# Kernel optimization log

Measured on AMD Instinct MI355X. Metric: run time of the kernel, lower is better.

The kernel has to match this reference:

```python
import jax, jax.numpy as jnp
import numpy as np

N = 64        # SSM state size
L = 4096      # sequence / kernel length (l_max)
BH = 4096     # batch * channels


def setup_inputs() -> dict:
    key = jax.random.key(0)
    ks = jax.random.split(key, 8)
    u = jax.random.normal(ks[0], (BH, L), dtype=jnp.float32)
    # S4D-Lin style eigenvalue init: Re = -0.5, Im = pi * n
    Lambda_re = -0.5 * jnp.ones((N,), dtype=jnp.float32)
    Lambda_im = jnp.pi * jnp.arange(N, dtype=jnp.float32)
    P_re = jax.random.normal(ks[1], (N,), dtype=jnp.float32) * (0.5 ** 0.5)
    P_im = jax.random.normal(ks[2], (N,), dtype=jnp.float32) * (0.5 ** 0.5)
    B_re = jax.random.normal(ks[3], (N,), dtype=jnp.float32)
    B_im = jax.random.normal(ks[4], (N,), dtype=jnp.float32)
    C_ri = jax.random.normal(ks[5], (N, 2), dtype=jnp.float32) * (0.5 ** 0.5)
    D = jnp.ones((1,), dtype=jnp.float32)
    # log_step ~ uniform(log(0.001), log(0.1)) as in log_step_initializer
    log_step = jax.random.uniform(ks[6], (1,), dtype=jnp.float32,
                                  minval=jnp.log(0.001), maxval=jnp.log(0.1))
    return {"u": u, "Lambda_re": Lambda_re, "Lambda_im": Lambda_im,
            "P_re": P_re, "P_im": P_im, "B_re": B_re, "B_im": B_im,
            "C_ri": C_ri, "D": D, "log_step": log_step}


def kernel_DPLR(Lambda, P, Q, B, C, step, length):
    # Evaluate the SSM generating function at the roots of unity via 4 Cauchy dots,
    # then inverse FFT to recover the length-L convolution kernel.
    Omega_L = jnp.exp((-2j * jnp.pi) * (jnp.arange(length) / length))  # (L,)
    a0, a1 = jnp.conj(C), jnp.conj(Q)
    b0, b1 = B, P
    g = (2.0 / step) * ((1.0 - Omega_L) / (1.0 + Omega_L))  # (L,)
    c = 2.0 / (1.0 + Omega_L)                               # (L,)

    def cauchy(v):  # v: (N,) -> (L,)
        return (v[None, :] / (g[:, None] - Lambda[None, :])).sum(-1)

    k00 = cauchy(a0 * b0)
    k01 = cauchy(a0 * b1)
    k10 = cauchy(a1 * b0)
    k11 = cauchy(a1 * b1)
    at_roots = c * (k00 - k01 * (1.0 / (1.0 + k11)) * k10)
    return jnp.fft.ifft(at_roots, length).real  # (L,)


def causal_convolution(u, K):
    # FFT-based linear (causal) convolution; u: (..., L), K: (L,)
    n = 2 * u.shape[-1]
    ud = jnp.fft.rfft(u, n=n, axis=-1)
    Kd = jnp.fft.rfft(K, n=n)
    return jnp.fft.irfft(ud * Kd, n=n, axis=-1)[..., : u.shape[-1]]


def reference(u, Lambda_re, Lambda_im, P_re, P_im, B_re, B_im, C_ri, D, log_step):
    Lambda = Lambda_re + 1j * Lambda_im
    P = P_re + 1j * P_im
    B = B_re + 1j * B_im
    C = C_ri[..., 0] + 1j * C_ri[..., 1]
    step = jnp.exp(log_step)  # (1,)
    K = kernel_DPLR(Lambda, P, P, B, C, step, u.shape[-1])  # (L,) real
    y_s = causal_convolution(u, K) + D * u  # (BH, L)
    return y_s
```

## Files before the change

### kernel.cpp

```cpp
#include <hip/hip_runtime.h>
#include <math.h>

#define LSEQ 4096
#define MFFT 8192
#define NM   64
#define NBH  4096

__device__ __forceinline__ float2 cmulf(float2 a, float2 b) {
  return make_float2(a.x*b.x - a.y*b.y, a.x*b.y + a.y*b.x);
}
__device__ __forceinline__ float2 cmulc(float2 a, float2 b) {
  return make_float2(a.x*b.x + a.y*b.y, a.y*b.x - a.x*b.y);
}
__device__ __forceinline__ float2 caddf(float2 a, float2 b){ return make_float2(a.x+b.x, a.y+b.y); }
__device__ __forceinline__ float2 csubf(float2 a, float2 b){ return make_float2(a.x-b.x, a.y-b.y); }

__device__ __forceinline__ int ZS(int i){ return i ^ ((i>>4)&15) ^ (((i>>8)&15)<<4); }

__device__ __forceinline__ void dft8_fwd(float2 x[8]) {
  const float RC = 0.7071067811865476f;
  float2 u0=caddf(x[0],x[4]), v0=csubf(x[0],x[4]);
  float2 u1=caddf(x[1],x[5]), d1=csubf(x[1],x[5]);
  float2 u2=caddf(x[2],x[6]), d2=csubf(x[2],x[6]);
  float2 u3=caddf(x[3],x[7]), d3=csubf(x[3],x[7]);
  float2 v1 = make_float2(RC*(d1.x + d1.y), RC*(d1.y - d1.x));
  float2 v2 = make_float2(d2.y, -d2.x);
  float2 v3 = make_float2(RC*(d3.y - d3.x), -RC*(d3.x + d3.y));
  float2 p0=caddf(u0,u2), q0=csubf(u0,u2);
  float2 p1=caddf(u1,u3), qt=csubf(u1,u3);
  float2 q1 = make_float2(qt.y, -qt.x);
  float2 r0=caddf(v0,v2), s0=csubf(v0,v2);
  float2 r1=caddf(v1,v3), st=csubf(v1,v3);
  float2 s1 = make_float2(st.y, -st.x);
  x[0]=caddf(p0,p1); x[4]=csubf(p0,p1);
  x[2]=caddf(q0,q1); x[6]=csubf(q0,q1);
  x[1]=caddf(r0,r1); x[5]=csubf(r0,r1);
  x[3]=caddf(s0,s1); x[7]=csubf(s0,s1);
}
__device__ __forceinline__ void dft8_inv(float2 x[8]) {
  const float RC = 0.7071067811865476f;
  float2 p0=caddf(x[0],x[4]), p1=csubf(x[0],x[4]);
  float2 q0=caddf(x[2],x[6]), q1=csubf(x[2],x[6]);
  float2 r0=caddf(x[1],x[5]), r1=csubf(x[1],x[5]);
  float2 s0=caddf(x[3],x[7]), s1=csubf(x[3],x[7]);
  float2 q1i = make_float2(-q1.y, q1.x);
  float2 s1i = make_float2(-s1.y, s1.x);
  float2 u0=caddf(p0,q0), u2=csubf(p0,q0);
  float2 u1=caddf(p1,q1i), u3=csubf(p1,q1i);
  float2 v0=caddf(r0,s0), v2=csubf(r0,s0);
  float2 v1=caddf(r1,s1i), v3=csubf(r1,s1i);
  float2 w1 = make_float2(RC*(v1.x - v1.y), RC*(v1.x + v1.y));
  float2 w2 = make_float2(-v2.y, v2.x);
  float2 w3 = make_float2(-RC*(v3.x + v3.y), RC*(v3.x - v3.y));
  x[0]=caddf(u0,v0); x[4]=csubf(u0,v0);
  x[1]=caddf(u1,w1); x[5]=csubf(u1,w1);
  x[2]=caddf(u2,w2); x[6]=csubf(u2,w2);
  x[3]=caddf(u3,w3); x[7]=csubf(u3,w3);
}

__device__ __forceinline__ void tw_fwd(float2 x[8], const float4* __restrict__ T, int J, int j) {
  float4 a0 = T[j],       a1 = T[J+j];
  x[1]=cmulf(x[1],make_float2(a0.x,a0.y));
  x[2]=cmulf(x[2],make_float2(a0.z,a0.w));
  x[3]=cmulf(x[3],make_float2(a1.x,a1.y));
  x[4]=cmulf(x[4],make_float2(a1.z,a1.w));
  float4 a2 = T[2*J+j],   a3 = T[3*J+j];
  x[5]=cmulf(x[5],make_float2(a2.x,a2.y));
  x[6]=cmulf(x[6],make_float2(a2.z,a2.w));
  x[7]=cmulf(x[7],make_float2(a3.x,a3.y));
}
__device__ __forceinline__ void tw_inv(float2 x[8], const float4* __restrict__ T, int J, int j) {
  float4 a0 = T[j],       a1 = T[J+j];
  x[1]=cmulc(x[1],make_float2(a0.x,a0.y));
  x[2]=cmulc(x[2],make_float2(a0.z,a0.w));
  x[3]=cmulc(x[3],make_float2(a1.x,a1.y));
  x[4]=cmulc(x[4],make_float2(a1.z,a1.w));
  float4 a2 = T[2*J+j],   a3 = T[3*J+j];
  x[5]=cmulc(x[5],make_float2(a2.x,a2.y));
  x[6]=cmulc(x[6],make_float2(a2.z,a2.w));
  x[7]=cmulc(x[7],make_float2(a3.x,a3.y));
}

#define DECL_W16C \
  const float2 W16C[8] = { make_float2(1.f,0.f), \
    make_float2(0.9238795325112867f,-0.3826834323650898f), \
    make_float2(0.7071067811865476f,-0.7071067811865476f), \
    make_float2(0.3826834323650898f,-0.9238795325112867f), \
    make_float2(0.f,-1.f), \
    make_float2(-0.3826834323650898f,-0.9238795325112867f), \
    make_float2(-0.7071067811865476f,-0.7071067811865476f), \
    make_float2(-0.9238795325112867f,-0.3826834323650898f) };

__device__ __forceinline__ float2 W8192e(long long e) {
  double ang = -2.0*M_PI*(double)(e & (MFFT-1))/(double)MFFT;
  return make_float2((float)cos(ang), (float)sin(ang));
}

__global__ void prep1_kernel(const float* __restrict__ Lre, const float* __restrict__ Lim,
                             const float* __restrict__ Pre, const float* __restrict__ Pim,
                             const float* __restrict__ Bre, const float* __restrict__ Bim,
                             const float* __restrict__ Cri, const float* __restrict__ lstep,
                             float2* __restrict__ a_out,
                             float4* __restrict__ T1, float4* __restrict__ T2,
                             float4* __restrict__ T3) {
  if (blockIdx.x >= 64) {
    int idx = (blockIdx.x - 64)*blockDim.x + threadIdx.x;
    if (idx < 4096) {
      int q = idx >> 10, j = idx & 1023;
      float2 wa = W8192e((long long)j*(2*q+1));
      float2 wb = W8192e((long long)j*(2*q+2));
      T1[(q<<10)+j] = make_float4(wa.x, wa.y, wb.x, wb.y);
    } else if (idx < 4608) {
      int r = idx - 4096; int q = r >> 7, j = r & 127;
      float2 wa = W8192e(8LL*j*(2*q+1));
      float2 wb = W8192e(8LL*j*(2*q+2));
      T2[(q<<7)+j] = make_float4(wa.x, wa.y, wb.x, wb.y);
    } else if (idx < 4672) {
      int r = idx - 4608; int q = r >> 4, j = r & 15;
      float2 wa = W8192e(64LL*j*(2*q+1));
      float2 wb = W8192e(64LL*j*(2*q+2));
      T3[(q<<4)+j] = make_float4(wa.x, wa.y, wb.x, wb.y);
    }
    return;
  }
  const int tid = threadIdx.x;
  const int k = (blockIdx.x << 6) + (tid >> 2);
  const int sub = tid & 3;
  double step = exp((double)lstep[0]);
  double ang = -2.0*M_PI*(double)k/(double)LSEQ;
  double wr = cos(ang), wi = sin(ang);
  double nr = 1.0 - wr, ni = -wi;
  double dr = 1.0 + wr, di = wi;
  double dn = dr*dr + di*di;
  double gre = (2.0/step) * (nr*dr + ni*di)/dn;
  double gim = (2.0/step) * (ni*dr - nr*di)/dn;
  double cre = 2.0*dr/dn, cim = -2.0*di/dn;
  double k00r=0,k00i=0,k01r=0,k01i=0,k10r=0,k10i=0,k11r=0,k11i=0;
  for (int n = sub; n < NM; n += 4) {
    double lre = Lre[n], lim = Lim[n];
    double pre = Pre[n], pim = Pim[n];
    double bre = Bre[n], bim = Bim[n];
    double ccr = Cri[2*n], cci = Cri[2*n+1];
    double er = gre - lre, ei = gim - lim;
    double inv = 1.0/(er*er + ei*ei);
    double ir =  er*inv, ii = -ei*inv;
    double v00r = ccr*bre + cci*bim, v00i = ccr*bim - cci*bre;
    double v01r = ccr*pre + cci*pim, v01i = ccr*pim - cci*pre;
    double v10r = pre*bre + pim*bim, v10i = pre*bim - pim*bre;
    double v11r = pre*pre + pim*pim, v11i = 0.0;
    k00r += v00r*ir - v00i*ii;  k00i += v00r*ii + v00i*ir;
    k01r += v01r*ir - v01i*ii;  k01i += v01r*ii + v01i*ir;
    k10r += v10r*ir - v10i*ii;  k10i += v10r*ii + v10i*ir;
    k11r += v11r*ir - v11i*ii;  k11i += v11r*ii + v11i*ir;
  }
  #pragma unroll
  for (int d = 1; d <= 2; d <<= 1) {
    k00r += __shfl_xor(k00r, d);  k00i += __shfl_xor(k00i, d);
    k01r += __shfl_xor(k01r, d);  k01i += __shfl_xor(k01i, d);
    k10r += __shfl_xor(k10r, d);  k10i += __shfl_xor(k10i, d);
    k11r += __shfl_xor(k11r, d);  k11i += __shfl_xor(k11i, d);
  }
  if (sub == 0) {
    double numr = k01r*k10r - k01i*k10i, numi = k01r*k10i + k01i*k10r;
    double der = 1.0 + k11r, dei = k11i;
    double dinv = 1.0/(der*der + dei*dei);
    double qr = (numr*der + numi*dei)*dinv;
    double qi = (numi*der - numr*dei)*dinv;
    double tr = k00r - qr, ti = k00i - qi;
    double ar = cre*tr - cim*ti, ai = cre*ti + cim*tr;
    a_out[k] = make_float2((float)ar, (float)ai);
  }
}

__global__ void ktime_kernel(const float2* __restrict__ a, float* __restrict__ K) {
  int lane = threadIdx.x & 63;
  int l = blockIdx.x * (blockDim.x >> 6) + (threadIdx.x >> 6);
  if (l >= LSEQ) return;
  double ang0 = 2.0*M_PI*(double)((l*lane) & (LSEQ-1))/(double)LSEQ;
  double tr = cos(ang0), ti = sin(ang0);
  double ang1 = 2.0*M_PI*(double)(l & 63)/64.0;
  double wr = cos(ang1), wi = sin(ang1);
  double acc = 0.0;
  for (int k = 0; k < 64; k++) {
    float2 ak = a[lane + (k << 6)];
    acc += (double)ak.x*tr - (double)ak.y*ti;
    double ntr = tr*wr - ti*wi;
    ti = tr*wi + ti*wr;
    tr = ntr;
  }
  for (int off = 32; off > 0; off >>= 1) acc += __shfl_down(acc, off);
  if (lane == 0) K[l] = (float)(acc/(double)LSEQ);
}

__global__ void kd8_kernel(const float* __restrict__ K, const float* __restrict__ Dp,
                           const float4* __restrict__ T1, const float4* __restrict__ T2,
                           const float4* __restrict__ T3,
                           float2* __restrict__ KdE, float2* __restrict__ KdO) {
  __shared__ float2 z[MFFT];
  const int t = threadIdx.x;
  float2 x[8];
  #pragma unroll
  for (int k = 0; k < 4; k++) {
    float v = K[t + (k<<10)];
    if (t == 0 && k == 0) v += Dp[0];
    x[k] = make_float2(v, 0.f);
  }
  #pragma unroll
  for (int k = 4; k < 8; k++) x[k] = make_float2(0.f, 0.f);
  dft8_fwd(x); tw_fwd(x, T1, 1024, t);
  #pragma unroll
  for (int m = 0; m < 8; m++) z[ZS(t + (m<<10))] = x[m];
  __syncthreads();
  {
    const int j2 = t & 127, gb2 = (t>>7)<<10;
    int ai[8];
    #pragma unroll
    for (int m = 0; m < 8; m++) ai[m] = ZS(gb2 + j2 + (m<<7));
    #pragma unroll
    for (int m = 0; m < 8; m++) x[m] = z[ai[m]];
    dft8_fwd(x); tw_fwd(x, T2, 128, j2);
    #pragma unroll
    for (int m = 0; m < 8; m++) z[ai[m]] = x[m];
  }
  __syncthreads();
  {
    const int j3 = t & 15, gb3 = (t>>4)<<7;
    int ai[8];
    #pragma unroll
    for (int m = 0; m < 8; m++) ai[m] = ZS(gb3 + j3 + (m<<4));
    #pragma unroll
    for (int m = 0; m < 8; m++) x[m] = z[ai[m]];
    dft8_fwd(x); tw_fwd(x, T3, 16, j3);
    #pragma unroll
    for (int m = 0; m < 8; m++) z[ai[m]] = x[m];
  }
  __builtin_amdgcn_wave_barrier();
  {
    DECL_W16C
    const int G4 = t>>1, j1 = t & 1, gb4 = G4<<4;
    #pragma unroll
    for (int m = 0; m < 8; m++) x[m] = z[ZS(gb4 + j1 + (m<<1))];
    dft8_fwd(x);
    #pragma unroll
    for (int m = 1; m < 8; m++) {
      float2 wm = j1 ? W16C[m] : make_float2(1.f, 0.f);
      x[m] = cmulf(x[m], wm);
    }
    const float sc = 1.0f/8192.0f;
    float2* kout = (j1 ? KdO : KdE) + (G4<<3);
    #pragma unroll
    for (int p = 0; p < 8; p++) {
      float ox = __shfl_xor(x[p].x, 1);
      float oy = __shfl_xor(x[p].y, 1);
      float2 v = j1 ? make_float2(ox - x[p].x, oy - x[p].y)
                    : make_float2(x[p].x + ox, x[p].y + oy);
      kout[p] = make_float2(v.x*sc, v.y*sc);
    }
  }
}

__global__ __launch_bounds__(1024, 4)
void conv8_kernel(const float* __restrict__ u,
                  const float4* __restrict__ T1, const float4* __restrict__ T2,
                  const float4* __restrict__ T3,
                  const float2* __restrict__ KdE, const float2* __restrict__ KdO,
                  float* __restrict__ out) {
  __shared__ float2 z[MFFT];
  const int t = threadIdx.x;
  const int r0 = blockIdx.x, r1 = blockIdx.x + (NBH/2);
  const float* u0 = u + (size_t)r0*LSEQ;
  const float* u1 = u + (size_t)r1*LSEQ;
  float2 x[8];
  {
    #pragma unroll
    for (int k = 0; k < 4; k++)
      x[k] = make_float2(u0[t + (k<<10)], u1[t + (k<<10)]);
    #pragma unroll
    for (int k = 4; k < 8; k++) x[k] = make_float2(0.f, 0.f);
    dft8_fwd(x); tw_fwd(x, T1, 1024, t);
    #pragma unroll
    for (int m = 0; m < 8; m++) z[ZS(t + (m<<10))] = x[m];
  }
  __syncthreads();
  const int j2 = t & 127, gb2 = (t>>7)<<10;
  {
    int ai[8];
    #pragma unroll
    for (int m = 0; m < 8; m++) ai[m] = ZS(gb2 + j2 + (m<<7));
    #pragma unroll
    for (int m = 0; m < 8; m++) x[m] = z[ai[m]];
    dft8_fwd(x); tw_fwd(x, T2, 128, j2);
    #pragma unroll
    for (int m = 0; m < 8; m++) z[ai[m]] = x[m];
  }
  __syncthreads();
  const int j3 = t & 15, gb3 = (t>>4)<<7;
  {
    int ai[8];
    #pragma unroll
    for (int m = 0; m < 8; m++) ai[m] = ZS(gb3 + j3 + (m<<4));
    #pragma unroll
    for (int m = 0; m < 8; m++) x[m] = z[ai[m]];
    dft8_fwd(x); tw_fwd(x, T3, 16, j3);
    #pragma unroll
    for (int m = 0; m < 8; m++) z[ai[m]] = x[m];
  }
  __builtin_amdgcn_wave_barrier();
  {
    DECL_W16C
    const int G4 = t>>1, j1 = t & 1, gb4 = G4<<4;
    int ai[8];
    #pragma unroll
    for (int m = 0; m < 8; m++) ai[m] = ZS(gb4 + j1 + (m<<1));
    #pragma unroll
    for (int m = 0; m < 8; m++) x[m] = z[ai[m]];
    dft8_fwd(x);
    #pragma unroll
    for (int m = 1; m < 8; m++) {
      float2 wm = j1 ? W16C[m] : make_float2(1.f, 0.f);
      x[m] = cmulf(x[m], wm);
    }
    const float4* kp = (const float4*)((j1 ? KdO : KdE) + (G4<<3));
    #pragma unroll
    for (int p2 = 0; p2 < 4; p2++) {
      float4 kq = kp[p2];
      #pragma unroll
      for (int s = 0; s < 2; s++) {
        const int p = 2*p2 + s;
        float2 kd = s ? make_float2(kq.z, kq.w) : make_float2(kq.x, kq.y);
        float ox = __shfl_xor(x[p].x, 1);
        float oy = __shfl_xor(x[p].y, 1);
        float2 v = j1 ? make_float2(ox - x[p].x, oy - x[p].y)
                      : make_float2(x[p].x + ox, x[p].y + oy);
        x[p] = cmulf(v, kd);
      }
    }
    #pragma unroll
    for (int p = 0; p < 8; p++) {
      float ox = __shfl_xor(x[p].x, 1);
      float oy = __shfl_xor(x[p].y, 1);
      x[p] = j1 ? make_float2(ox - x[p].x, oy - x[p].y)
                : make_float2(x[p].x + ox, x[p].y + oy);
    }
    #pragma unroll
    for (int m = 1; m < 8; m++) {
      float2 wm = j1 ? W16C[m] : make_float2(1.f, 0.f);
      x[m] = cmulc(x[m], wm);
    }
    dft8_inv(x);
    #pragma unroll
    for (int m = 0; m < 8; m++) z[ai[m]] = x[m];
  }
  __builtin_amdgcn_wave_barrier();
  {
    int ai[8];
    #pragma unroll
    for (int m = 0; m < 8; m++) ai[m] = ZS(gb3 + j3 + (m<<4));
    #pragma unroll
    for (int m = 0; m < 8; m++) x[m] = z[ai[m]];
    tw_inv(x, T3, 16, j3); dft8_inv(x);
    #pragma unroll
    for (int m = 0; m < 8; m++) z[ai[m]] = x[m];
  }
  __syncthreads();
  {
    int ai[8];
    #pragma unroll
    for (int m = 0; m < 8; m++) ai[m] = ZS(gb2 + j2 + (m<<7));
    #pragma unroll
    for (int m = 0; m < 8; m++) x[m] = z[ai[m]];
    tw_inv(x, T2, 128, j2); dft8_inv(x);
    #pragma unroll
    for (int m = 0; m < 8; m++) z[ai[m]] = x[m];
  }
  __syncthreads();
  {
    #pragma unroll
    for (int m = 0; m < 8; m++) x[m] = z[ZS(t + (m<<10))];
    tw_inv(x, T1, 1024, t); dft8_inv(x);
    float* o0 = out + (size_t)r0*LSEQ;
    float* o1 = out + (size_t)r1*LSEQ;
    #pragma unroll
    for (int m = 0; m < 4; m++) {
      int idx = t + (m<<10);
      o0[idx] = x[m].x;
      o1[idx] = x[m].y;
    }
  }
}

extern "C" void kernel_launch(void* const* d_in, const int* in_sizes, int n_in,
                              void* d_out, int out_size, void* d_ws, size_t ws_size,
                              hipStream_t stream) {
  const float* u     = (const float*)d_in[0];
  const float* Lre   = (const float*)d_in[1];
  const float* Lim   = (const float*)d_in[2];
  const float* Pre   = (const float*)d_in[3];
  const float* Pim   = (const float*)d_in[4];
  const float* Bre   = (const float*)d_in[5];
  const float* Bim   = (const float*)d_in[6];
  const float* Cri   = (const float*)d_in[7];
  const float* Dp    = (const float*)d_in[8];
  const float* lstep = (const float*)d_in[9];
  float* out = (float*)d_out;

  char* ws = (char*)d_ws;
  float2* a_ws   = (float2*)(ws);
  float*  K_ws   = (float*)(ws + 32768);
  float2* KdE_ws = (float2*)(ws + 49152);
  float2* KdO_ws = (float2*)(ws + 81920);
  float4* T1_ws  = (float4*)(ws + 114688);
  float4* T2_ws  = (float4*)(ws + 180224);
  float4* T3_ws  = (float4*)(ws + 188416);

  hipLaunchKernelGGL(prep1_kernel,  dim3(83),   dim3(256), 0, stream,
                     Lre, Lim, Pre, Pim, Bre, Bim, Cri, lstep, a_ws,
                     T1_ws, T2_ws, T3_ws);
  hipLaunchKernelGGL(ktime_kernel,  dim3(1024), dim3(256), 0, stream, a_ws, K_ws);
  hipLaunchKernelGGL(kd8_kernel,    dim3(1),    dim3(1024), 0, stream,
                     K_ws, Dp, T1_ws, T2_ws, T3_ws, KdE_ws, KdO_ws);
  hipLaunchKernelGGL(conv8_kernel,  dim3(NBH/2), dim3(1024), 0, stream,
                     u, T1_ws, T2_ws, T3_ws, KdE_ws, KdO_ws, out);
}
```

Baseline: 104.9 us.

## Use half-length complex FFT with real-signal packing for causal convolution

Replaces the 8192-point complex FFT that packed two rows as real and imaginary parts with a 4096-point complex FFT per row, which treats the length-8192 real zero-padded signal as 4096 complex samples. Even/odd spectrum separation and recombination happen in the middle, using mirrored shared-memory reads and precomputed twiddle and mirror tables. The kernel spectrum is now computed by a direct DFT kernel plus a remapping kernel instead of the single-block FFT. This halves shared memory per block and uses more blocks with fewer threads each, at the cost of extra pointwise arithmetic, gather reads and two added small launches.

```diff
diff --git a/kernel.cpp b/kernel.cpp
--- a/kernel.cpp
+++ b/kernel.cpp
@@ -2,7 +2,7 @@
 #include <math.h>
 
 #define LSEQ 4096
-#define MFFT 8192
+#define NC   4096
 #define NM   64
 #define NBH  4096
 
@@ -15,7 +15,11 @@
 __device__ __forceinline__ float2 caddf(float2 a, float2 b){ return make_float2(a.x+b.x, a.y+b.y); }
 __device__ __forceinline__ float2 csubf(float2 a, float2 b){ return make_float2(a.x-b.x, a.y-b.y); }
 
-__device__ __forceinline__ int ZS(int i){ return i ^ ((i>>4)&15) ^ (((i>>8)&15)<<4); }
+__host__ __device__ __forceinline__ int rev3(int x){ return ((x&7)<<6) | (x&56) | ((x>>6)&7); }
+
+__device__ __forceinline__ int ZS4(int i){
+  return i ^ ((i>>3)&7) ^ (((i>>6)&7)<<3);
+}
 
 __device__ __forceinline__ void dft8_fwd(float2 x[8]) {
   const float RC = 0.7071067811865476f;
@@ -92,7 +96,7 @@
     make_float2(-0.9238795325112867f,-0.3826834323650898f) };
 
 __device__ __forceinline__ float2 W8192e(long long e) {
-  double ang = -2.0*M_PI*(double)(e & (MFFT-1))/(double)MFFT;
+  double ang = -2.0*M_PI*(double)(e & 8191)/8192.0;
   return make_float2((float)cos(ang), (float)sin(ang));
 }
 
@@ -102,24 +106,30 @@
                              const float* __restrict__ Cri, const float* __restrict__ lstep,
                              float2* __restrict__ a_out,
                              float4* __restrict__ T1, float4* __restrict__ T2,
-                             float4* __restrict__ T3) {
+                             float4* __restrict__ T3, float2* __restrict__ wb,
+                             int* __restrict__ mir) {
   if (blockIdx.x >= 64) {
     int idx = (blockIdx.x - 64)*blockDim.x + threadIdx.x;
-    if (idx < 4096) {
-      int q = idx >> 10, j = idx & 1023;
-      float2 wa = W8192e((long long)j*(2*q+1));
-      float2 wb = W8192e((long long)j*(2*q+2));
-      T1[(q<<10)+j] = make_float4(wa.x, wa.y, wb.x, wb.y);
-    } else if (idx < 4608) {
-      int r = idx - 4096; int q = r >> 7, j = r & 127;
-      float2 wa = W8192e(8LL*j*(2*q+1));
-      float2 wb = W8192e(8LL*j*(2*q+2));
-      T2[(q<<7)+j] = make_float4(wa.x, wa.y, wb.x, wb.y);
-    } else if (idx < 4672) {
-      int r = idx - 4608; int q = r >> 4, j = r & 15;
-      float2 wa = W8192e(64LL*j*(2*q+1));
-      float2 wb = W8192e(64LL*j*(2*q+2));
-      T3[(q<<4)+j] = make_float4(wa.x, wa.y, wb.x, wb.y);
+    if (idx < 2048) {
+      int q = idx >> 9, j = idx & 511;
+      float2 wa = W8192e(2LL*j*(2*q+1));
+      float2 wbv = W8192e(2LL*j*(2*q+2));
+      T1[(q<<9)+j] = make_float4(wa.x, wa.y, wbv.x, wbv.y);
+    } else if (idx < 2304) {
+      int r = idx - 2048; int q = r >> 6, j = r & 63;
+      float2 wa = W8192e(16LL*j*(2*q+1));
+      float2 wbv = W8192e(16LL*j*(2*q+2));
+      T2[(q<<6)+j] = make_float4(wa.x, wa.y, wbv.x, wbv.y);
+    } else if (idx < 2336) {
+      int r = idx - 2304; int q = r >> 3, j = r & 7;
+      float2 wa = W8192e(128LL*j*(2*q+1));
+      float2 wbv = W8192e(128LL*j*(2*q+2));
+      T3[(q<<3)+j] = make_float4(wa.x, wa.y, wbv.x, wbv.y);
+    } else if (idx < 2848) {
+      int t = idx - 2336;
+      int r = rev3(t);
+      wb[t] = W8192e((long long)r);
+      mir[t] = (r == 0) ? 0 : rev3(512 - r);
     }
     return;
   }
@@ -192,200 +202,151 @@
   if (lane == 0) K[l] = (float)(acc/(double)LSEQ);
 }
 
-__global__ void kd8_kernel(const float* __restrict__ K, const float* __restrict__ Dp,
-                           const float4* __restrict__ T1, const float4* __restrict__ T2,
-                           const float4* __restrict__ T3,
-                           float2* __restrict__ KdE, float2* __restrict__ KdO) {
-  __shared__ float2 z[MFFT];
-  const int t = threadIdx.x;
+__global__ void hspec_kernel(const float* __restrict__ K, float2* __restrict__ H) {
+  int lane = threadIdx.x & 63;
+  int k = blockIdx.x * (blockDim.x >> 6) + (threadIdx.x >> 6);
+  if (k > NC) return;
+  int m0 = (k*lane) & 8191;
+  double a0 = -2.0*M_PI*(double)m0/8192.0;
+  double cr = cos(a0), ci = sin(a0);
+  int ms = (k << 6) & 8191;
+  double as = -2.0*M_PI*(double)ms/8192.0;
+  double sr = cos(as), si = sin(as);
+  double accr = 0.0, acci = 0.0;
+  for (int j = 0; j < 64; j++) {
+    double Kv = (double)K[lane + (j << 6)];
+    accr += Kv*cr; acci += Kv*ci;
+    double nr2 = cr*sr - ci*si;
+    ci = cr*si + ci*sr; cr = nr2;
+  }
+  for (int off = 32; off > 0; off >>= 1) {
+    accr += __shfl_down(accr, off);
+    acci += __shfl_down(acci, off);
+  }
+  if (lane == 0) H[k] = make_float2((float)accr, (float)acci);
+}
+
+__global__ void kdmap_kernel(const float2* __restrict__ H, const float* __restrict__ Dp,
+                             float2* __restrict__ kda, float2* __restrict__ kdb) {
+  int p = blockIdx.x*blockDim.x + threadIdx.x;
+  if (p >= NC) return;
+  int k = ((p & 7) << 9) | rev3(p >> 3);
+  const float s = 1.0f/16384.0f;
+  float Dv = Dp[0];
+  float2 ha = H[k], hb = H[NC - k];
+  kda[p] = make_float2((ha.x + Dv)*s, ha.y*s);
+  kdb[p] = make_float2((hb.x + Dv)*s, hb.y*s);
+}
+
+__global__ __launch_bounds__(512, 4)
+void conv4_kernel(const float* __restrict__ u,
+                  const float4* __restrict__ T1, const float4* __restrict__ T2,
+                  const float4* __restrict__ T3, const float2* __restrict__ wbt,
+                  const int* __restrict__ mir, const float2* __restrict__ kda,
+                  const float2* __restrict__ kdb, float* __restrict__ out) {
+  __shared__ float2 z[NC];
+  const int T = threadIdx.x;
+  const float2* u2 = (const float2*)(u + (size_t)blockIdx.x*LSEQ);
   float2 x[8];
-  #pragma unroll
-  for (int k = 0; k < 4; k++) {
-    float v = K[t + (k<<10)];
-    if (t == 0 && k == 0) v += Dp[0];
-    x[k] = make_float2(v, 0.f);
-  }
-  #pragma unroll
-  for (int k = 4; k < 8; k++) x[k] = make_float2(0.f, 0.f);
-  dft8_fwd(x); tw_fwd(x, T1, 1024, t);
-  #pragma unroll
-  for (int m = 0; m < 8; m++) z[ZS(t + (m<<10))] = x[m];
+  {
+    #pragma unroll
+    for (int m = 0; m < 4; m++) x[m] = u2[T + (m<<9)];
+    #pragma unroll
+    for (int m = 4; m < 8; m++) x[m] = make_float2(0.f, 0.f);
+    dft8_fwd(x); tw_fwd(x, T1, 512, T);
+    #pragma unroll
+    for (int m = 0; m < 8; m++) z[ZS4(T + (m<<9))] = x[m];
+  }
   __syncthreads();
-  {
-    const int j2 = t & 127, gb2 = (t>>7)<<10;
-    int ai[8];
-    #pragma unroll
-    for (int m = 0; m < 8; m++) ai[m] = ZS(gb2 + j2 + (m<<7));
-    #pragma unroll
-    for (int m = 0; m < 8; m++) x[m] = z[ai[m]];
-    dft8_fwd(x); tw_fwd(x, T2, 128, j2);
-    #pragma unroll
-    for (int m = 0; m < 8; m++) z[ai[m]] = x[m];
+  const int j2 = T & 63, g2 = (T>>6)<<9;
+  {
+    #pragma unroll
+    for (int m = 0; m < 8; m++) x[m] = z[ZS4(g2 + j2 + (m<<6))];
+    dft8_fwd(x); tw_fwd(x, T2, 64, j2);
+    #pragma unroll
+    for (int m = 0; m < 8; m++) z[ZS4(g2 + j2 + (m<<6))] = x[m];
+  }
+  __builtin_amdgcn_wave_barrier();
+  const int j3 = T & 7, g3 = (T>>3)<<6;
+  {
+    #pragma unroll
+    for (int m = 0; m < 8; m++) x[m] = z[ZS4(g3 + j3 + (m<<3))];
+    dft8_fwd(x); tw_fwd(x, T3, 8, j3);
+    #pragma unroll
+    for (int m = 0; m < 8; m++) z[ZS4(g3 + j3 + (m<<3))] = x[m];
+  }
+  __builtin_amdgcn_wave_barrier();
+  {
+    #pragma unroll
+    for (int m = 0; m < 8; m++) x[m] = z[ZS4((T<<3) + m)];
+    dft8_fwd(x);
+    #pragma unroll
+    for (int m = 0; m < 8; m++) z[ZS4((T<<3) + m)] = x[m];
   }
   __syncthreads();
   {
-    const int j3 = t & 15, gb3 = (t>>4)<<7;
-    int ai[8];
-    #pragma unroll
-    for (int m = 0; m < 8; m++) ai[m] = ZS(gb3 + j3 + (m<<4));
-    #pragma unroll
-    for (int m = 0; m < 8; m++) x[m] = z[ai[m]];
-    dft8_fwd(x); tw_fwd(x, T3, 16, j3);
-    #pragma unroll
-    for (int m = 0; m < 8; m++) z[ai[m]] = x[m];
-  }
-  __builtin_amdgcn_wave_barrier();
-  {
     DECL_W16C
-    const int G4 = t>>1, j1 = t & 1, gb4 = G4<<4;
-    #pragma unroll
-    for (int m = 0; m < 8; m++) x[m] = z[ZS(gb4 + j1 + (m<<1))];
-    dft8_fwd(x);
-    #pragma unroll
-    for (int m = 1; m < 8; m++) {
-      float2 wm = j1 ? W16C[m] : make_float2(1.f, 0.f);
-      x[m] = cmulf(x[m], wm);
-    }
-    const float sc = 1.0f/8192.0f;
-    float2* kout = (j1 ? KdO : KdE) + (G4<<3);
-    #pragma unroll
-    for (int p = 0; p < 8; p++) {
-      float ox = __shfl_xor(x[p].x, 1);
-      float oy = __shfl_xor(x[p].y, 1);
-      float2 v = j1 ? make_float2(ox - x[p].x, oy - x[p].y)
-                    : make_float2(x[p].x + ox, x[p].y + oy);
-      kout[p] = make_float2(v.x*sc, v.y*sc);
-    }
-  }
-}
-
-__global__ __launch_bounds__(1024, 4)
-void conv8_kernel(const float* __restrict__ u,
-                  const float4* __restrict__ T1, const float4* __restrict__ T2,
-                  const float4* __restrict__ T3,
-                  const float2* __restrict__ KdE, const float2* __restrict__ KdO,
-                  float* __restrict__ out) {
-  __shared__ float2 z[MFFT];
-  const int t = threadIdx.x;
-  const int r0 = blockIdx.x, r1 = blockIdx.x + (NBH/2);
-  const float* u0 = u + (size_t)r0*LSEQ;
-  const float* u1 = u + (size_t)r1*LSEQ;
-  float2 x[8];
-  {
-    #pragma unroll
-    for (int k = 0; k < 4; k++)
-      x[k] = make_float2(u0[t + (k<<10)], u1[t + (k<<10)]);
-    #pragma unroll
-    for (int k = 4; k < 8; k++) x[k] = make_float2(0.f, 0.f);
-    dft8_fwd(x); tw_fwd(x, T1, 1024, t);
-    #pragma unroll
-    for (int m = 0; m < 8; m++) z[ZS(t + (m<<10))] = x[m];
-  }
-  __syncthreads();
-  const int j2 = t & 127, gb2 = (t>>7)<<10;
-  {
-    int ai[8];
-    #pragma unroll
-    for (int m = 0; m < 8; m++) ai[m] = ZS(gb2 + j2 + (m<<7));
-    #pragma unroll
-    for (int m = 0; m < 8; m++) x[m] = z[ai[m]];
-    dft8_fwd(x); tw_fwd(x, T2, 128, j2);
-    #pragma unroll
-    for (int m = 0; m < 8; m++) z[ai[m]] = x[m];
-  }
-  __syncthreads();
-  const int j3 = t & 15, gb3 = (t>>4)<<7;
-  {
-    int ai[8];
-    #pragma unroll
-    for (int m = 0; m < 8; m++) ai[m] = ZS(gb3 + j3 + (m<<4));
-    #pragma unroll
-    for (int m = 0; m < 8; m++) x[m] = z[ai[m]];
-    dft8_fwd(x); tw_fwd(x, T3, 16, j3);
-    #pragma unroll
-    for (int m = 0; m < 8; m++) z[ai[m]] = x[m];
-  }
-  __builtin_amdgcn_wave_barrier();
-  {
-    DECL_W16C
-    const int G4 = t>>1, j1 = t & 1, gb4 = G4<<4;
-    int ai[8];
-    #pragma unroll
-    for (int m = 0; m < 8; m++) ai[m] = ZS(gb4 + j1 + (m<<1));
-    #pragma unroll
-    for (int m = 0; m < 8; m++) x[m] = z[ai[m]];
-    dft8_fwd(x);
-    #pragma unroll
-    for (int m = 1; m < 8; m++) {
-      float2 wm = j1 ? W16C[m] : make_float2(1.f, 0.f);
-      x[m] = cmulf(x[m], wm);
-    }
-    const float4* kp = (const float4*)((j1 ? KdO : KdE) + (G4<<3));
+    const float2 wbase = wbt[T];
+    const int tp = mir[T];
+    const bool t0 = (T == 0);
+    const float4* ka4 = (const float4*)(kda + (T<<3));
+    const float4* kb4 = (const float4*)(kdb + (T<<3));
     #pragma unroll
     for (int p2 = 0; p2 < 4; p2++) {
-      float4 kq = kp[p2];
+      float4 a4 = ka4[p2], b4 = kb4[p2];
       #pragma unroll
       for (int s = 0; s < 2; s++) {
-        const int p = 2*p2 + s;
-        float2 kd = s ? make_float2(kq.z, kq.w) : make_float2(kq.x, kq.y);
-        float ox = __shfl_xor(x[p].x, 1);
-        float oy = __shfl_xor(x[p].y, 1);
-        float2 v = j1 ? make_float2(ox - x[p].x, oy - x[p].y)
-                      : make_float2(x[p].x + ox, x[p].y + oy);
-        x[p] = cmulf(v, kd);
+        const int m = 2*p2 + s;
+        float2 kdaV = s ? make_float2(a4.z, a4.w) : make_float2(a4.x, a4.y);
+        float2 kdbV = s ? make_float2(b4.z, b4.w) : make_float2(b4.x, b4.y);
+        const int mp = t0 ? ((8 - m) & 7) : (7 - m);
+        float2 Zm = z[ZS4((tp<<3) + mp)];
+        float2 Zo = x[m];
+        float2 wk = cmulf(wbase, W16C[m]);
+        float Sx = Zo.x + Zm.x, Sy = Zo.y - Zm.y;
+        float Dx = Zo.x - Zm.x, Dy = Zo.y + Zm.y;
+        float2 t1 = cmulf(wk, make_float2(Dx, Dy));
+        float2 Up = make_float2(Sx + t1.y, Sy - t1.x);
+        float2 Um = make_float2(Sx - t1.y, -Sy - t1.x);
+        float2 Yp = cmulf(Up, kdaV);
+        float2 Ym = cmulf(Um, kdbV);
+        float Pxx = Yp.x + Ym.x, Pyy = Yp.y - Ym.y;
+        float Qx  = Yp.x - Ym.x, Qy  = Yp.y + Ym.y;
+        float2 t2 = cmulc(make_float2(Qx, Qy), wk);
+        x[m] = make_float2(Pxx - t2.y, Pyy + t2.x);
       }
     }
-    #pragma unroll
-    for (int p = 0; p < 8; p++) {
-      float ox = __shfl_xor(x[p].x, 1);
-      float oy = __shfl_xor(x[p].y, 1);
-      x[p] = j1 ? make_float2(ox - x[p].x, oy - x[p].y)
-                : make_float2(x[p].x + ox, x[p].y + oy);
-    }
-    #pragma unroll
-    for (int m = 1; m < 8; m++) {
-      float2 wm = j1 ? W16C[m] : make_float2(1.f, 0.f);
-      x[m] = cmulc(x[m], wm);
-    }
+  }
+  __syncthreads();
+  {
     dft8_inv(x);
     #pragma unroll
-    for (int m = 0; m < 8; m++) z[ai[m]] = x[m];
+    for (int m = 0; m < 8; m++) z[ZS4((T<<3) + m)] = x[m];
   }
   __builtin_amdgcn_wave_barrier();
   {
-    int ai[8];
-    #pragma unroll
-    for (int m = 0; m < 8; m++) ai[m] = ZS(gb3 + j3 + (m<<4));
-    #pragma unroll
-    for (int m = 0; m < 8; m++) x[m] = z[ai[m]];
-    tw_inv(x, T3, 16, j3); dft8_inv(x);
-    #pragma unroll
-    for (int m = 0; m < 8; m++) z[ai[m]] = x[m];
+    #pragma unroll
+    for (int m = 0; m < 8; m++) x[m] = z[ZS4(g3 + j3 + (m<<3))];
+    tw_inv(x, T3, 8, j3); dft8_inv(x);
+    #pragma unroll
+    for (int m = 0; m < 8; m++) z[ZS4(g3 + j3 + (m<<3))] = x[m];
+  }
+  __builtin_amdgcn_wave_barrier();
+  {
+    #pragma unroll
+    for (int m = 0; m < 8; m++) x[m] = z[ZS4(g2 + j2 + (m<<6))];
+    tw_inv(x, T2, 64, j2); dft8_inv(x);
+    #pragma unroll
+    for (int m = 0; m < 8; m++) z[ZS4(g2 + j2 + (m<<6))] = x[m];
   }
   __syncthreads();
   {
-    int ai[8];
-    #pragma unroll
-    for (int m = 0; m < 8; m++) ai[m] = ZS(gb2 + j2 + (m<<7));
-    #pragma unroll
-    for (int m = 0; m < 8; m++) x[m] = z[ai[m]];
-    tw_inv(x, T2, 128, j2); dft8_inv(x);
-    #pragma unroll
-    for (int m = 0; m < 8; m++) z[ai[m]] = x[m];
-  }
-  __syncthreads();
-  {
-    #pragma unroll
-    for (int m = 0; m < 8; m++) x[m] = z[ZS(t + (m<<10))];
-    tw_inv(x, T1, 1024, t); dft8_inv(x);
-    float* o0 = out + (size_t)r0*LSEQ;
-    float* o1 = out + (size_t)r1*LSEQ;
-    #pragma unroll
-    for (int m = 0; m < 4; m++) {
-      int idx = t + (m<<10);
-      o0[idx] = x[m].x;
-      o1[idx] = x[m].y;
-    }
+    #pragma unroll
+    for (int m = 0; m < 8; m++) x[m] = z[ZS4(T + (m<<9))];
+    tw_inv(x, T1, 512, T); dft8_inv(x);
+    float2* o2 = (float2*)(out + (size_t)blockIdx.x*LSEQ);
+    #pragma unroll
+    for (int m = 0; m < 4; m++) o2[T + (m<<9)] = x[m];
   }
 }
 
@@ -407,18 +368,22 @@
   char* ws = (char*)d_ws;
   float2* a_ws   = (float2*)(ws);
   float*  K_ws   = (float*)(ws + 32768);
-  float2* KdE_ws = (float2*)(ws + 49152);
-  float2* KdO_ws = (float2*)(ws + 81920);
-  float4* T1_ws  = (float4*)(ws + 114688);
-  float4* T2_ws  = (float4*)(ws + 180224);
-  float4* T3_ws  = (float4*)(ws + 188416);
-
-  hipLaunchKernelGGL(prep1_kernel,  dim3(83),   dim3(256), 0, stream,
+  float2* kdb_ws = (float2*)(ws + 49152);
+  float2* H_ws   = (float2*)(ws + 81920);
+  float4* T1_ws  = (float4*)(ws + 115072);
+  float4* T2_ws  = (float4*)(ws + 147840);
+  float4* T3_ws  = (float4*)(ws + 151936);
+  float2* wb_ws  = (float2*)(ws + 152448);
+  int*    mir_ws = (int*)(ws + 156544);
+  float2* kda_ws = a_ws;
+
+  hipLaunchKernelGGL(prep1_kernel, dim3(76),   dim3(256), 0, stream,
                      Lre, Lim, Pre, Pim, Bre, Bim, Cri, lstep, a_ws,
-                     T1_ws, T2_ws, T3_ws);
-  hipLaunchKernelGGL(ktime_kernel,  dim3(1024), dim3(256), 0, stream, a_ws, K_ws);
-  hipLaunchKernelGGL(kd8_kernel,    dim3(1),    dim3(1024), 0, stream,
-                     K_ws, Dp, T1_ws, T2_ws, T3_ws, KdE_ws, KdO_ws);
-  hipLaunchKernelGGL(conv8_kernel,  dim3(NBH/2), dim3(1024), 0, stream,
-                     u, T1_ws, T2_ws, T3_ws, KdE_ws, KdO_ws, out);
-}
+                     T1_ws, T2_ws, T3_ws, wb_ws, mir_ws);
+  hipLaunchKernelGGL(ktime_kernel, dim3(1024), dim3(256), 0, stream, a_ws, K_ws);
+  hipLaunchKernelGGL(hspec_kernel, dim3(1025), dim3(256), 0, stream, K_ws, H_ws);
+  hipLaunchKernelGGL(kdmap_kernel, dim3(16),   dim3(256), 0, stream,
+                     H_ws, Dp, kda_ws, kdb_ws);
+  hipLaunchKernelGGL(conv4_kernel, dim3(NBH),  dim3(512), 0, stream,
+                     u, T1_ws, T2_ws, T3_ws, wb_ws, mir_ws, kda_ws, kdb_ws, out);
+}
```

After: 162.9 us. +55.2%, slower.
